# Optimization experiments

Measured on AMD Instinct MI355X. Metric: run time of the kernel, lower is better.

## Reference

```python
import jax, jax.numpy as jnp
import numpy as np

B, N, D = 2, 2048, 1024
H, WS = 16, 128  # num_heads, window_size
DH = D // H
HALF = WS // 2  # window is [i-HALF, i+HALF] inclusive -> 129 keys interior


def setup_inputs() -> dict:
    key = jax.random.key(0)
    ks = jax.random.split(key, 5)
    return {
        "x": jax.random.normal(ks[0], (B, N, D), dtype=jnp.float32),
        "Wqkv": jax.random.normal(ks[1], (D, 3 * D), dtype=jnp.float32) * 0.02,
        "bqkv": jax.random.normal(ks[2], (3 * D,), dtype=jnp.float32) * 0.02,
        "Wout": jax.random.normal(ks[3], (D, D), dtype=jnp.float32) * 0.02,
        "bout": jax.random.normal(ks[4], (D,), dtype=jnp.float32) * 0.02,
    }


def reference(x, Wqkv, bqkv, Wout, bout):
    b, n, d = x.shape
    scale = DH ** -0.5
    qkv = x @ Wqkv + bqkv  # [b, n, 3d]
    q, k, v = jnp.split(qkv, 3, axis=-1)
    # [b, n, d] -> [b, h, n, dh]
    def heads(t):
        return t.reshape(b, n, H, DH).transpose(0, 2, 1, 3)
    q, k, v = heads(q), heads(k), heads(v)
    scores = jnp.einsum("bhid,bhjd->bhij", q, k) * scale  # [b, h, n, n]
    # per-token window [max(0,i-HALF), min(n,i+HALF+1)) == |i-j| <= HALF
    idx = jnp.arange(n)
    band = jnp.abs(idx[:, None] - idx[None, :]) <= HALF  # [n, n]
    neg = jnp.asarray(jnp.finfo(scores.dtype).min, scores.dtype)
    scores = jnp.where(band[None, None], scores, neg)
    attn = jax.nn.softmax(scores, axis=-1)
    out = jnp.einsum("bhij,bhjd->bhid", attn, v)  # [b, h, n, dh]
    out = out.transpose(0, 2, 1, 3).reshape(b, n, d)
    return out @ Wout + bout
```

## Files before the change

kernel.cpp:

```cpp
#include <hip/hip_runtime.h>
#include <hip/hip_bf16.h>
#include <cstdint>
#include <cstddef>

#define BB 2
#define NN 2048
#define DD 1024
#define HH 16
#define DHH 64
#define SCALE 0.125f

typedef _Float16 f16x8 __attribute__((ext_vector_type(8)));
typedef _Float16 f16x4 __attribute__((ext_vector_type(4)));
typedef float f32x4 __attribute__((ext_vector_type(4)));

#define AS1(p) ((__attribute__((address_space(1))) void*)(p))
#define AS3(p) ((__attribute__((address_space(3))) void*)(p))

__global__ __launch_bounds__(256) void prep(const float* __restrict__ x, _Float16* __restrict__ x_h,
                                            const float* __restrict__ Wqkv, _Float16* __restrict__ Wqkv_t,
                                            const float* __restrict__ Wout, _Float16* __restrict__ Wout_t) {
    __shared__ float tile[32][33];
    int bx = blockIdx.x, tid = threadIdx.x;
    if (bx < 2048) {
        int i = bx * 2048 + tid * 8;
        f32x4 a = *(const f32x4*)(x + i);
        f32x4 b = *(const f32x4*)(x + i + 4);
        f16x8 o;
        o[0] = (_Float16)a[0]; o[1] = (_Float16)a[1]; o[2] = (_Float16)a[2]; o[3] = (_Float16)a[3];
        o[4] = (_Float16)b[0]; o[5] = (_Float16)b[1]; o[6] = (_Float16)b[2]; o[7] = (_Float16)b[3];
        *(f16x8*)(x_h + i) = o;
        return;
    }
    const float* in; _Float16* out; int C, tc, tr;
    if (bx < 5120) { int t = bx - 2048; C = 3 * DD; in = Wqkv; out = Wqkv_t; tc = t % 96; tr = t / 96; }
    else           { int t = bx - 5120; C = DD;     in = Wout; out = Wout_t; tc = t % 32; tr = t / 32; }
    int R = DD;
    int txx = tid & 31, ty = tid >> 5;
    int r0 = tr * 32, c0 = tc * 32;
#pragma unroll
    for (int i = 0; i < 32; i += 8)
        tile[ty + i][txx] = in[(size_t)(r0 + ty + i) * C + (c0 + txx)];
    __syncthreads();
#pragma unroll
    for (int i = 0; i < 32; i += 8)
        out[(size_t)(c0 + ty + i) * R + (r0 + txx)] = (_Float16)tile[txx][ty + i];
}

template <int BM>
__global__ __launch_bounds__(256) void gemm_f16_bt(const _Float16* __restrict__ A,
                                                   const _Float16* __restrict__ Bt,
                                                   const float* __restrict__ bias,
                                                   _Float16* __restrict__ Ch,
                                                   float* __restrict__ Cf,
                                                   int M, int N, int K) {
    constexpr int MT = BM / 32;
    constexpr int AP = BM / 32;
    __shared__ __align__(16) _Float16 As[BM * 64];
    __shared__ __align__(16) _Float16 Bs[128 * 64];
    int tid = threadIdx.x;
    int wave = tid >> 6, lane = tid & 63;
    int bm = blockIdx.y * BM, bn = blockIdx.x * 128;
    int wm = (wave >> 1) * (BM / 2), wn = (wave & 1) * 64;
    int lhi = lane >> 4, llo = lane & 15;

    f32x4 acc[MT][4] = {};

    int srowA = wave * (BM / 4) + (lane >> 3);
    int srowB = wave * 32 + (lane >> 3);
    int scol = ((lane & 7) ^ (lane >> 3)) * 8;
    const _Float16* gA = A + (size_t)(bm + srowA) * K + scol;
    const _Float16* gB = Bt + (size_t)(bn + srowB) * K + scol;
    _Float16* lA = As + wave * (AP * 512) + lane * 8;
    _Float16* lB = Bs + wave * 2048 + lane * 8;

    for (int k0 = 0; k0 < K; k0 += 64) {
        __syncthreads();
#pragma unroll
        for (int p = 0; p < AP; ++p)
            __builtin_amdgcn_global_load_lds(AS1(gA + (size_t)p * 8 * K + k0), AS3(lA + p * 512), 16, 0, 0);
#pragma unroll
        for (int p = 0; p < 4; ++p)
            __builtin_amdgcn_global_load_lds(AS1(gB + (size_t)p * 8 * K + k0), AS3(lB + p * 512), 16, 0, 0);
        __syncthreads();

#pragma unroll
        for (int ks = 0; ks < 2; ++ks) {
            f16x8 af[MT], bf[4];
            int swz = (((ks * 4 + lhi) ^ (llo & 7)) * 8);
#pragma unroll
            for (int mt = 0; mt < MT; ++mt)
                af[mt] = *(const f16x8*)(As + (wm + mt * 16 + llo) * 64 + swz);
#pragma unroll
            for (int nt = 0; nt < 4; ++nt)
                bf[nt] = *(const f16x8*)(Bs + (wn + nt * 16 + llo) * 64 + swz);
#pragma unroll
            for (int mt = 0; mt < MT; ++mt)
#pragma unroll
                for (int nt = 0; nt < 4; ++nt)
                    acc[mt][nt] = __builtin_amdgcn_mfma_f32_16x16x32_f16(af[mt], bf[nt], acc[mt][nt], 0, 0, 0);
        }
    }

#pragma unroll
    for (int nt = 0; nt < 4; ++nt) {
        int col = bn + wn + nt * 16 + llo;
        float bv = bias[col];
#pragma unroll
        for (int mt = 0; mt < MT; ++mt) {
#pragma unroll
            for (int r = 0; r < 4; ++r) {
                int row = bm + wm + mt * 16 + lhi * 4 + r;
                float v = acc[mt][nt][r] + bv;
                if (Ch) Ch[(size_t)row * N + col] = (_Float16)v;
                else    Cf[(size_t)row * N + col] = v;
            }
        }
    }
}

#define KP 64
#define PP 200
#define VP 200
__global__ __launch_bounds__(256) void local_attn(const _Float16* __restrict__ qkv,
                                                  _Float16* __restrict__ outh) {
    __shared__ __align__(16) _Float16 Ks[192 * KP];
    __shared__ __align__(16) _Float16 Ps[64 * PP];
    __shared__ __align__(16) _Float16 Vt[64 * VP];
    int tid = threadIdx.x;
    int i0 = blockIdx.x * 64;
    int h = blockIdx.y, b = blockIdx.z;
    const ptrdiff_t rs = 3 * DD;
    const _Float16* base = qkv + (ptrdiff_t)(b * NN) * rs + h * DHH;

    int wave = tid >> 6, lane = tid & 63;
    int llo = lane & 15, lhi = lane >> 4;

    {
        int srow = lane >> 3;
        int chunk = ((lane & 7) ^ (lane >> 3)) * 8;
#pragma unroll
        for (int q = 0; q < 6; ++q) {
            int p = wave * 6 + q;
            int j = i0 - 64 + p * 8 + srow;
            const _Float16* g = base + (ptrdiff_t)j * rs + DD + chunk;
            __builtin_amdgcn_global_load_lds(AS1(g), AS3(Ks + p * 512 + lane * 8), 16, 0, 0);
        }
    }

    for (int u = tid; u < 1536; u += 256) {
        int s = u >> 3, d8c = u & 7, d8 = d8c * 8;
        int j = i0 - 64 + s;
        f16x8 vv = {0,0,0,0,0,0,0,0};
        if (j >= 0 && j < NN)
            vv = *(const f16x8*)(base + (ptrdiff_t)j * rs + 2 * DD + d8);
#pragma unroll
        for (int i = 0; i < 8; ++i) {
            int t = (i + d8c) & 7;
            Vt[(d8 + t) * VP + s] = vv[t];
        }
    }

    int qrow = wave * 16 + llo;
    int qi = i0 + qrow;
    const _Float16* qp = base + (ptrdiff_t)qi * rs;
    f16x8 qf0 = *(const f16x8*)(qp + lhi * 8);
    f16x8 qf1 = *(const f16x8*)(qp + 32 + lhi * 8);
    __syncthreads();

    float sc[12][4];
#pragma unroll
    for (int mt = 0; mt < 12; ++mt) {
        const _Float16* kr = Ks + (mt * 16 + llo) * 64;
        f16x8 kf0 = *(const f16x8*)(kr + ((lhi ^ (llo & 7)) * 8));
        f16x8 kf1 = *(const f16x8*)(kr + (((lhi + 4) ^ (llo & 7)) * 8));
        f32x4 a = {0.f, 0.f, 0.f, 0.f};
        a = __builtin_amdgcn_mfma_f32_16x16x32_f16(kf0, qf0, a, 0, 0, 0);
        a = __builtin_amdgcn_mfma_f32_16x16x32_f16(kf1, qf1, a, 0, 0, 0);
#pragma unroll
        for (int r = 0; r < 4; ++r) sc[mt][r] = a[r];
    }

    float m = -1e30f;
#pragma unroll
    for (int mt = 0; mt < 12; ++mt)
#pragma unroll
        for (int r = 0; r < 4; ++r) {
            int sidx = mt * 16 + lhi * 4 + r;
            int j = i0 - 64 + sidx;
            int dj = j - qi;
            bool valid = (j >= 0) && (j < NN) && (dj <= 64) && (dj >= -64);
            float v = valid ? sc[mt][r] * SCALE : -1e30f;
            sc[mt][r] = v;
            m = fmaxf(m, v);
        }
    m = fmaxf(m, __shfl_xor(m, 16, 64));
    m = fmaxf(m, __shfl_xor(m, 32, 64));
    float l = 0.f;
#pragma unroll
    for (int mt = 0; mt < 12; ++mt)
#pragma unroll
        for (int r = 0; r < 4; ++r) {
            float e = __expf(sc[mt][r] - m);
            sc[mt][r] = e;
            l += e;
        }
    l += __shfl_xor(l, 16, 64);
    l += __shfl_xor(l, 32, 64);
    float invl = 1.f / l;

#pragma unroll
    for (int mt = 0; mt < 12; ++mt) {
        f16x4 pv;
#pragma unroll
        for (int r = 0; r < 4; ++r) pv[r] = (_Float16)(sc[mt][r] * invl);
        *(f16x4*)(Ps + qrow * PP + mt * 16 + lhi * 4) = pv;
    }
    __asm__ volatile("s_waitcnt lgkmcnt(0)" ::: "memory");

    f32x4 oacc[4] = {};
#pragma unroll
    for (int ks = 0; ks < 6; ++ks) {
        f16x8 pf = *(const f16x8*)(Ps + (wave * 16 + llo) * PP + ks * 32 + lhi * 8);
#pragma unroll
        for (int nt = 0; nt < 4; ++nt) {
            f16x8 vf = *(const f16x8*)(Vt + (nt * 16 + llo) * VP + ks * 32 + lhi * 8);
            oacc[nt] = __builtin_amdgcn_mfma_f32_16x16x32_f16(pf, vf, oacc[nt], 0, 0, 0);
        }
    }

    _Float16* orow = outh + (size_t)(b * NN) * DD + h * DHH;
#pragma unroll
    for (int nt = 0; nt < 4; ++nt)
#pragma unroll
        for (int r = 0; r < 4; ++r) {
            int q = wave * 16 + lhi * 4 + r;
            int d = nt * 16 + llo;
            orow[(size_t)(i0 + q) * DD + d] = (_Float16)oacc[nt][r];
        }
}

extern "C" void kernel_launch(void* const* d_in, const int* in_sizes, int n_in,
                              void* d_out, int out_size, void* d_ws, size_t ws_size,
                              hipStream_t stream) {
    const float* x    = (const float*)d_in[0];
    const float* Wqkv = (const float*)d_in[1];
    const float* bqkv = (const float*)d_in[2];
    const float* Wout = (const float*)d_in[3];
    const float* bout = (const float*)d_in[4];
    float* out = (float*)d_out;

    char* ws = (char*)d_ws;
    _Float16* x_h    = (_Float16*)(ws);
    _Float16* Wqkv_t = (_Float16*)(ws + (size_t)8  * 1024 * 1024);
    _Float16* Wout_t = (_Float16*)(ws + (size_t)14 * 1024 * 1024);
    _Float16* qkv_h  = (_Float16*)(ws + (size_t)16 * 1024 * 1024);
    _Float16* attn_h = (_Float16*)(ws + (size_t)40 * 1024 * 1024);

    int M = BB * NN;

    prep<<<6144, 256, 0, stream>>>(x, x_h, Wqkv, Wqkv_t, Wout, Wout_t);

    gemm_f16_bt<128><<<dim3((3 * DD) / 128, M / 128), 256, 0, stream>>>(
        x_h, Wqkv_t, bqkv, qkv_h, nullptr, M, 3 * DD, DD);

    local_attn<<<dim3(NN / 64, HH, BB), 256, 0, stream>>>(qkv_h, attn_h);

    gemm_f16_bt<64><<<dim3(DD / 128, M / 64), 256, 0, stream>>>(
        attn_h, Wout_t, bout, nullptr, out, M, DD, DD);
}
```

Before: 159.5 us.

## Emit separate Q, K and per-head transposed V from QKV GEMM epilogue

The QKV projection epilogue now writes Q and K into separate [B*N, D] buffers and V directly in a per-head transposed [B, H, DH, N] layout. The attention kernel can then fill its V^T shared-memory tile with contiguous 16-byte loads and stores. This replaces the earlier per-element scatter into LDS and its strided reads of the fused qkv buffer. In exchange, the V epilogue does transposed 4-element stores. The boundary zero-fill for out-of-range window rows is gone, so edge blocks now read neighbouring memory that the softmax masks out.

Result: no change. 162.5 us (+1.9%).

```diff
diff --git a/kernel.cpp b/kernel.cpp
--- a/kernel.cpp
+++ b/kernel.cpp
@@ -47,11 +47,88 @@
         out[(size_t)(c0 + ty + i) * R + (r0 + txx)] = (_Float16)tile[txx][ty + i];
 }
 
+__global__ __launch_bounds__(256) void gemm_qkv(const _Float16* __restrict__ A,
+                                                const _Float16* __restrict__ Bt,
+                                                const float* __restrict__ bias,
+                                                _Float16* __restrict__ q_h,
+                                                _Float16* __restrict__ k_h,
+                                                _Float16* __restrict__ vt_h) {
+    const int K = DD, M = BB * NN;
+    __shared__ __align__(16) _Float16 As[128 * 64];
+    __shared__ __align__(16) _Float16 Bs[128 * 64];
+    int tid = threadIdx.x;
+    int wave = tid >> 6, lane = tid & 63;
+    int bm = blockIdx.y * 128, bn = blockIdx.x * 128;
+    int wm = (wave >> 1) * 64, wn = (wave & 1) * 64;
+    int lhi = lane >> 4, llo = lane & 15;
+    (void)M;
+
+    f32x4 acc[4][4] = {};
+
+    int srow = wave * 32 + (lane >> 3);
+    int scol = ((lane & 7) ^ (lane >> 3)) * 8;
+    const _Float16* gA = A + (size_t)(bm + srow) * K + scol;
+    const _Float16* gB = Bt + (size_t)(bn + srow) * K + scol;
+    _Float16* lA = As + wave * 2048 + lane * 8;
+    _Float16* lB = Bs + wave * 2048 + lane * 8;
+
+    for (int k0 = 0; k0 < K; k0 += 64) {
+        __syncthreads();
+#pragma unroll
+        for (int p = 0; p < 4; ++p) {
+            __builtin_amdgcn_global_load_lds(AS1(gA + (size_t)p * 8 * K + k0), AS3(lA + p * 512), 16, 0, 0);
+            __builtin_amdgcn_global_load_lds(AS1(gB + (size_t)p * 8 * K + k0), AS3(lB + p * 512), 16, 0, 0);
+        }
+        __syncthreads();
+
+#pragma unroll
+        for (int ks = 0; ks < 2; ++ks) {
+            f16x8 af[4], bf[4];
+            int swz = (((ks * 4 + lhi) ^ (llo & 7)) * 8);
+#pragma unroll
+            for (int mt = 0; mt < 4; ++mt)
+                af[mt] = *(const f16x8*)(As + (wm + mt * 16 + llo) * 64 + swz);
+#pragma unroll
+            for (int nt = 0; nt < 4; ++nt)
+                bf[nt] = *(const f16x8*)(Bs + (wn + nt * 16 + llo) * 64 + swz);
+#pragma unroll
+            for (int mt = 0; mt < 4; ++mt)
+#pragma unroll
+                for (int nt = 0; nt < 4; ++nt)
+                    acc[mt][nt] = __builtin_amdgcn_mfma_f32_16x16x32_f16(af[mt], bf[nt], acc[mt][nt], 0, 0, 0);
+        }
+    }
+
+    int region = bn >> 10;
+#pragma unroll
+    for (int nt = 0; nt < 4; ++nt) {
+        int col = bn + wn + nt * 16 + llo;
+        float bv = bias[col];
+        int c = col & 1023;
+#pragma unroll
+        for (int mt = 0; mt < 4; ++mt) {
+            int row = bm + wm + mt * 16 + lhi * 4;
+            int b = row >> 11, n = row & 2047;
+            if (region == 2) {
+                int h = c >> 6, dh = c & 63;
+                f16x4 v4;
+#pragma unroll
+                for (int r = 0; r < 4; ++r) v4[r] = (_Float16)(acc[mt][nt][r] + bv);
+                *(f16x4*)(vt_h + ((size_t)((b * HH + h) * DHH + dh)) * NN + n) = v4;
+            } else {
+                _Float16* dst = (region == 0 ? q_h : k_h) + ((size_t)(b * NN + n)) * DD + c;
+#pragma unroll
+                for (int r = 0; r < 4; ++r)
+                    dst[(size_t)r * DD] = (_Float16)(acc[mt][nt][r] + bv);
+            }
+        }
+    }
+}
+
 template <int BM>
 __global__ __launch_bounds__(256) void gemm_f16_bt(const _Float16* __restrict__ A,
                                                    const _Float16* __restrict__ Bt,
                                                    const float* __restrict__ bias,
-                                                   _Float16* __restrict__ Ch,
                                                    float* __restrict__ Cf,
                                                    int M, int N, int K) {
     constexpr int MT = BM / 32;
@@ -111,9 +188,7 @@
 #pragma unroll
             for (int r = 0; r < 4; ++r) {
                 int row = bm + wm + mt * 16 + lhi * 4 + r;
-                float v = acc[mt][nt][r] + bv;
-                if (Ch) Ch[(size_t)row * N + col] = (_Float16)v;
-                else    Cf[(size_t)row * N + col] = v;
+                Cf[(size_t)row * N + col] = acc[mt][nt][r] + bv;
             }
         }
     }
@@ -122,7 +197,9 @@
 #define KP 64
 #define PP 200
 #define VP 200
-__global__ __launch_bounds__(256) void local_attn(const _Float16* __restrict__ qkv,
+__global__ __launch_bounds__(256) void local_attn(const _Float16* __restrict__ q_h,
+                                                  const _Float16* __restrict__ k_h,
+                                                  const _Float16* __restrict__ vt_h,
                                                   _Float16* __restrict__ outh) {
     __shared__ __align__(16) _Float16 Ks[192 * KP];
     __shared__ __align__(16) _Float16 Ps[64 * PP];
@@ -130,8 +207,6 @@
     int tid = threadIdx.x;
     int i0 = blockIdx.x * 64;
     int h = blockIdx.y, b = blockIdx.z;
-    const ptrdiff_t rs = 3 * DD;
-    const _Float16* base = qkv + (ptrdiff_t)(b * NN) * rs + h * DHH;
 
     int wave = tid >> 6, lane = tid & 63;
     int llo = lane & 15, lhi = lane >> 4;
@@ -139,31 +214,27 @@
     {
         int srow = lane >> 3;
         int chunk = ((lane & 7) ^ (lane >> 3)) * 8;
+        const _Float16* kb = k_h + (size_t)(b * NN) * DD + h * DHH + chunk;
 #pragma unroll
         for (int q = 0; q < 6; ++q) {
             int p = wave * 6 + q;
             int j = i0 - 64 + p * 8 + srow;
-            const _Float16* g = base + (ptrdiff_t)j * rs + DD + chunk;
-            __builtin_amdgcn_global_load_lds(AS1(g), AS3(Ks + p * 512 + lane * 8), 16, 0, 0);
-        }
-    }
-
-    for (int u = tid; u < 1536; u += 256) {
-        int s = u >> 3, d8c = u & 7, d8 = d8c * 8;
-        int j = i0 - 64 + s;
-        f16x8 vv = {0,0,0,0,0,0,0,0};
-        if (j >= 0 && j < NN)
-            vv = *(const f16x8*)(base + (ptrdiff_t)j * rs + 2 * DD + d8);
-#pragma unroll
-        for (int i = 0; i < 8; ++i) {
-            int t = (i + d8c) & 7;
-            Vt[(d8 + t) * VP + s] = vv[t];
+            __builtin_amdgcn_global_load_lds(AS1(kb + (ptrdiff_t)j * DD), AS3(Ks + p * 512 + lane * 8), 16, 0, 0);
+        }
+    }
+
+    {
+        const _Float16* vb = vt_h + (size_t)((b * HH + h) * DHH) * NN + (i0 - 64);
+        for (int u = tid; u < 1536; u += 256) {
+            int d = u / 24, c = u % 24;
+            f16x8 vv = *(const f16x8*)(vb + (ptrdiff_t)d * NN + c * 8);
+            *(f16x8*)(Vt + d * VP + c * 8) = vv;
         }
     }
 
     int qrow = wave * 16 + llo;
     int qi = i0 + qrow;
-    const _Float16* qp = base + (ptrdiff_t)qi * rs;
+    const _Float16* qp = q_h + (size_t)(b * NN + qi) * DD + h * DHH;
     f16x8 qf0 = *(const f16x8*)(qp + lhi * 8);
     f16x8 qf1 = *(const f16x8*)(qp + 32 + lhi * 8);
     __syncthreads();
@@ -254,18 +325,20 @@
     _Float16* x_h    = (_Float16*)(ws);
     _Float16* Wqkv_t = (_Float16*)(ws + (size_t)8  * 1024 * 1024);
     _Float16* Wout_t = (_Float16*)(ws + (size_t)14 * 1024 * 1024);
-    _Float16* qkv_h  = (_Float16*)(ws + (size_t)16 * 1024 * 1024);
+    _Float16* q_h    = (_Float16*)(ws + (size_t)16 * 1024 * 1024);
+    _Float16* k_h    = (_Float16*)(ws + (size_t)24 * 1024 * 1024);
+    _Float16* vt_h   = (_Float16*)(ws + (size_t)32 * 1024 * 1024);
     _Float16* attn_h = (_Float16*)(ws + (size_t)40 * 1024 * 1024);
 
     int M = BB * NN;
 
     prep<<<6144, 256, 0, stream>>>(x, x_h, Wqkv, Wqkv_t, Wout, Wout_t);
 
-    gemm_f16_bt<128><<<dim3((3 * DD) / 128, M / 128), 256, 0, stream>>>(
-        x_h, Wqkv_t, bqkv, qkv_h, nullptr, M, 3 * DD, DD);
-
-    local_attn<<<dim3(NN / 64, HH, BB), 256, 0, stream>>>(qkv_h, attn_h);
+    gemm_qkv<<<dim3((3 * DD) / 128, M / 128), 256, 0, stream>>>(
+        x_h, Wqkv_t, bqkv, q_h, k_h, vt_h);
+
+    local_attn<<<dim3(NN / 64, HH, BB), 256, 0, stream>>>(q_h, k_h, vt_h, attn_h);
 
     gemm_f16_bt<64><<<dim3(DD / 128, M / 64), 256, 0, stream>>>(
-        attn_h, Wout_t, bout, nullptr, out, M, DD, DD);
-}
+        attn_h, Wout_t, bout, out, M, DD, DD);
+}
```
